# Kernel tuning notes

Hardware: AMD Instinct MI355X
Metric: run time of the kernel (lower is better)

The kernel has to match this reference:

```python
import jax, jax.numpy as jnp
import numpy as np

H = 16          # n_self_heads
CHUNK = 256     # chunk_size in chunk_gate_retention
GLN = 16.0      # gate_logit_normalizer
EPS = 1e-5      # norm_eps


def _rope_interleaved(t, cos, sin):
    # t: [B,T,H,hd]; cos,sin: [T,hd//2]; interleaved pairs (even, odd)
    x1 = t[..., 0::2]
    x2 = t[..., 1::2]
    c = cos[None, :, None, :]
    s = sin[None, :, None, :]
    r1 = x1 * c - x2 * s
    r2 = x1 * s + x2 * c
    return jnp.stack([r1, r2], axis=-1).reshape(t.shape)


def setup_inputs() -> dict:
    key = jax.random.key(0)
    ks = jax.random.split(key, 8)
    B, T, D = 2, 4096, 2048
    hd = D // H
    sc = D ** -0.5
    x = jax.random.normal(ks[0], (B, T, D), jnp.float32)
    # real rotary tables (interleaved), [T, hd//2]
    inv_freq = 1.0 / (10000.0 ** (np.arange(0, hd, 2, dtype=np.float32) / hd))
    ang = np.outer(np.arange(T, dtype=np.float32), inv_freq)
    cos = jnp.asarray(np.cos(ang))
    sin = jnp.asarray(np.sin(ang))
    Wq = jax.random.normal(ks[1], (D, D), jnp.float32) * sc
    Wk = jax.random.normal(ks[2], (D, D), jnp.float32) * sc
    Wv = jax.random.normal(ks[3], (D, D), jnp.float32) * sc
    Wg = jax.random.normal(ks[4], (D, D), jnp.float32) * sc
    Wgt = jax.random.normal(ks[5], (D, H), jnp.float32) * sc
    Wout = jax.random.normal(ks[6], (D, D), jnp.float32) * sc
    return {"x": x, "cos": cos, "sin": sin, "Wq": Wq, "Wk": Wk, "Wv": Wv,
            "Wg": Wg, "Wgt": Wgt, "Wout": Wout}


def reference(x, cos, sin, Wq, Wk, Wv, Wg, Wgt, Wout):
    B, T, D = x.shape
    hd = D // H
    N = T // CHUNK
    scale = hd ** -0.5

    q = (x @ Wq).reshape(B, T, H, hd)
    k = (x @ Wk).reshape(B, T, H, hd)
    v = (x @ Wv).reshape(B, T, H, hd)
    g = x @ Wg                                   # [B,T,D] swiglu gate
    gt = jax.nn.log_sigmoid(x @ Wgt) / GLN       # [B,T,H] log-decay per head

    q = _rope_interleaved(q, cos, sin)
    k = _rope_interleaved(k, cos, sin)

    # chunk: [B,H,N,C,hd]
    def chunked(t):
        return t.transpose(0, 2, 1, 3).reshape(B, H, N, CHUNK, hd)
    qc, kc, vc = chunked(q), chunked(k), chunked(v)

    gtc = gt.transpose(0, 2, 1).reshape(B, H, N, CHUNK).astype(jnp.float32)
    gcum = jnp.cumsum(gtc, axis=-1)              # inclusive cumsum within chunk

    # intra-chunk: A[i,j] = (q_i.k_j)*scale * exp(gcum_i - gcum_j), j <= i
    mask = jnp.tril(jnp.ones((CHUNK, CHUNK), bool))
    dec = jnp.where(mask, jnp.exp(gcum[..., :, None] - gcum[..., None, :]), 0.0).astype(x.dtype)
    scores = jnp.einsum('bhncd,bhnsd->bhncs', qc * scale, kc) * dec
    o_inner = jnp.einsum('bhncs,bhnsd->bhncd', scores, vc)

    # cross-chunk recurrent state: S <- S*exp(g_total) + (k*exp(g_total-gcum))^T V * scale
    g_tot = gcum[..., -1:]                       # [B,H,N,1]
    k_dec = jnp.exp(g_tot - gcum).astype(x.dtype)
    S_in = jnp.einsum('bhncd,bhnce->bhnde', kc * k_dec[..., None] * scale, vc)  # [B,H,N,hd,hd]
    q_dec = jnp.exp(gcum).astype(x.dtype)        # [B,H,N,C]
    chunk_dec = jnp.exp(gcum[..., -1]).astype(x.dtype)  # [B,H,N]

    def step(S, inp):
        qcn, qd, Sin, cd = inp
        o_cross = jnp.einsum('bhcd,bhde->bhce', qcn * qd[..., None], S)
        S_new = S * cd[..., None, None] + Sin
        return S_new, o_cross

    xs = (jnp.moveaxis(qc, 2, 0), jnp.moveaxis(q_dec, 2, 0),
          jnp.moveaxis(S_in, 2, 0), jnp.moveaxis(chunk_dec, 2, 0))
    S0 = jnp.zeros((B, H, hd, hd), x.dtype)
    _, o_cross = jax.lax.scan(step, S0, xs)      # [N,B,H,C,hd]

    o = o_inner + jnp.moveaxis(o_cross, 0, 2)    # [B,H,N,C,hd]
    # RMSNorm over head_dim, no affine
    o = o * jax.lax.rsqrt(jnp.mean(o * o, axis=-1, keepdims=True) + EPS)
    o = o.reshape(B, H, T, hd).transpose(0, 2, 1, 3).reshape(B, T, D)
    o = jax.nn.silu(g) * o                       # swiglu(g, o)
    return o @ Wout
```

## Files before the change

kernel.cpp:

```cpp
#include <hip/hip_runtime.h>

typedef unsigned short u16;
typedef short bf16x8 __attribute__((ext_vector_type(8)));
typedef unsigned short u16x8 __attribute__((ext_vector_type(8)));
typedef unsigned short u16x4 __attribute__((ext_vector_type(4)));
typedef float f32x4 __attribute__((ext_vector_type(4)));

typedef __attribute__((address_space(1))) void* gas_ptr;
typedef __attribute__((address_space(3))) void* las_ptr;

__device__ __forceinline__ float bf2f(u16 v) {
  unsigned u = ((unsigned)v) << 16;
  return __builtin_bit_cast(float, u);
}
__device__ __forceinline__ u16 f2bf(float f) {
  unsigned u = __builtin_bit_cast(unsigned, f);
  u += 0x7fffu + ((u >> 16) & 1u);
  return (u16)(u >> 16);
}
__device__ __forceinline__ f32x4 mfma16(bf16x8 a, bf16x8 b, f32x4 c) {
  return __builtin_amdgcn_mfma_f32_16x16x32_bf16(a, b, c, 0, 0, 0);
}
__device__ __forceinline__ void gload_lds16(const void* g, void* l) {
  __builtin_amdgcn_global_load_lds((gas_ptr)g, (las_ptr)l, 16, 0, 0);
}

#define SB __builtin_amdgcn_sched_barrier(0)
#define BAR do { SB; __builtin_amdgcn_s_barrier(); SB; } while (0)

__global__ void k_cast(const float* __restrict__ in, u16* __restrict__ out, int n8) {
  int stride = gridDim.x * blockDim.x;
  for (int i = blockIdx.x * blockDim.x + threadIdx.x; i < n8; i += stride) {
    size_t base = (size_t)i * 8;
    f32x4 a = *(const f32x4*)(in + base);
    f32x4 b = *(const f32x4*)(in + base + 4);
    u16x8 o;
    o[0] = f2bf(a[0]); o[1] = f2bf(a[1]); o[2] = f2bf(a[2]); o[3] = f2bf(a[3]);
    o[4] = f2bf(b[0]); o[5] = f2bf(b[1]); o[6] = f2bf(b[2]); o[7] = f2bf(b[3]);
    *(u16x8*)(out + base) = o;
  }
}

__global__ __launch_bounds__(256) void k_wtrans5(const float* __restrict__ W0,
                                                 const float* __restrict__ W1,
                                                 const float* __restrict__ W2,
                                                 const float* __restrict__ W3,
                                                 const float* __restrict__ W4,
                                                 u16* __restrict__ WT) {
  const int K = 2048, N = 2048;
  int z = blockIdx.z;
  const float* W = (z == 0) ? W0 : (z == 1) ? W1 : (z == 2) ? W2 : (z == 3) ? W3 : W4;
  u16* dst = WT + (size_t)z * 4194304;
  int n0 = blockIdx.x * 64, k0 = blockIdx.y * 64;
  int tid = threadIdx.x;
  __shared__ __align__(16) float tf[64][68];
  int r = tid >> 4, c4 = (tid & 15) * 4;
#pragma unroll
  for (int i = 0; i < 4; ++i) {
    int row = r + i * 16;
    f32x4 v = *(const f32x4*)(W + (size_t)(k0 + row) * N + n0 + c4);
    *(f32x4*)&tf[row][c4] = v;
  }
  __syncthreads();
#pragma unroll
  for (int i = 0; i < 2; ++i) {
    int chunk = tid + i * 256;
    int nl = chunk >> 3, c8 = (chunk & 7) * 8;
    u16x8 o;
#pragma unroll
    for (int m = 0; m < 8; ++m) o[m] = f2bf(tf[c8 + m][nl]);
    *(u16x8*)(dst + (size_t)(n0 + nl) * K + k0 + c8) = o;
  }
}

template <int MODE>
__global__ __launch_bounds__(512, 2) void k_gemm2(const u16* __restrict__ A,
                                                  const u16* __restrict__ Bt,
                                                  void* __restrict__ Cp, int M, int N, int K) {
  __shared__ __align__(16) u16 Al[2][2][8192];
  __shared__ __align__(16) u16 Bl[2][2][8192];
  int tid = threadIdx.x, w = tid >> 6, lane = tid & 63, l15 = lane & 15, l4 = lane >> 4;
  int wm = w >> 2, wn = w & 3;
  int nwg = gridDim.x, bid = blockIdx.x;
  int q8 = nwg >> 3;
  int wg = (bid & 7) * q8 + (bid >> 3);
  int nbx = N >> 8;
  int nstx = nbx >> 2;
  int st = wg >> 4, r16 = wg & 15;
  int sm = st / nstx, sn = st - sm * nstx;
  int m0 = ((sm << 2) + (r16 >> 2)) << 8;
  int n0 = ((sn << 2) + (r16 & 3)) << 8;
  int rA0, rA1, rB0, rB1, cc0, cc1;
  {
    int rr[2], cch[2];
#pragma unroll
    for (int q = 0; q < 2; ++q) {
      int L = (q * 512 + tid) * 16;
      int sub = L >> 10, inner = L & 1023;
      inner ^= ((inner >> 9) & 1) << 5;
      rr[q] = ((sub >> 1) << 4) + (inner >> 6);
      cch[q] = ((sub & 1) << 5) + ((inner & 63) >> 1);
    }
    rA0 = ((rr[0] >> 6) << 7) + (rr[0] & 63);
    rA1 = ((rr[1] >> 6) << 7) + (rr[1] & 63);
    rB0 = ((rr[0] >> 5) << 6) + (rr[0] & 31);
    rB1 = ((rr[1] >> 5) << 6) + (rr[1] & 31);
    cc0 = cch[0]; cc1 = cch[1];
  }
  int innerA = ((l15 << 6) + (l4 << 4)) ^ ((l15 & 8) << 2);
  int ldsW = w << 9;

#define STAGE_A(t, h)                                                                   \
  do {                                                                                  \
    int b_ = (t) & 1;                                                                   \
    gload_lds16(A + (size_t)(m0 + rA0 + (h) * 64) * K + (t) * 64 + cc0, &Al[b_][h][ldsW]); \
    gload_lds16(A + (size_t)(m0 + rA1 + (h) * 64) * K + (t) * 64 + cc1, &Al[b_][h][4096 + ldsW]); \
  } while (0)
#define STAGE_B(t, h)                                                                   \
  do {                                                                                  \
    int b_ = (t) & 1;                                                                   \
    gload_lds16(Bt + (size_t)(n0 + rB0 + (h) * 32) * K + (t) * 64 + cc0, &Bl[b_][h][ldsW]); \
    gload_lds16(Bt + (size_t)(n0 + rB1 + (h) * 32) * K + (t) * 64 + cc1, &Bl[b_][h][4096 + ldsW]); \
  } while (0)

  const f32x4 z4 = {0.f, 0.f, 0.f, 0.f};
  f32x4 acc[8][4];
#pragma unroll
  for (int i = 0; i < 8; ++i)
#pragma unroll
    for (int j = 0; j < 4; ++j) acc[i][j] = z4;
  bf16x8 af0[4][2], af1[4][2], bf0[2][2], bf1[2][2];

#define LDA0(buf)                                                                        \
  do {                                                                                   \
    const char* Ab = (const char*)&Al[buf][0][0];                                        \
    _Pragma("unroll") for (int fi = 0; fi < 4; ++fi) _Pragma("unroll") for (int ks = 0; ks < 2; ++ks) \
        af0[fi][ks] = *(const bf16x8*)(Ab + (((wm * 4 + fi) * 2 + ks) << 10) + innerA);  \
  } while (0)
#define LDA1(buf)                                                                        \
  do {                                                                                   \
    const char* Ab = (const char*)&Al[buf][1][0];                                        \
    _Pragma("unroll") for (int fi = 0; fi < 4; ++fi) _Pragma("unroll") for (int ks = 0; ks < 2; ++ks) \
        af1[fi][ks] = *(const bf16x8*)(Ab + (((wm * 4 + fi) * 2 + ks) << 10) + innerA);  \
  } while (0)
#define LDB0(buf)                                                                        \
  do {                                                                                   \
    const char* Bb = (const char*)&Bl[buf][0][0];                                        \
    _Pragma("unroll") for (int fj = 0; fj < 2; ++fj) _Pragma("unroll") for (int ks = 0; ks < 2; ++ks) \
        bf0[fj][ks] = *(const bf16x8*)(Bb + (((wn * 2 + fj) * 2 + ks) << 10) + innerA);  \
  } while (0)
#define LDB1(buf)                                                                        \
  do {                                                                                   \
    const char* Bb = (const char*)&Bl[buf][1][0];                                        \
    _Pragma("unroll") for (int fj = 0; fj < 2; ++fj) _Pragma("unroll") for (int ks = 0; ks < 2; ++ks) \
        bf1[fj][ks] = *(const bf16x8*)(Bb + (((wn * 2 + fj) * 2 + ks) << 10) + innerA);  \
  } while (0)
#define MM(hm, hn, AF, BF)                                                               \
  do {                                                                                   \
    __builtin_amdgcn_s_setprio(1);                                                       \
    _Pragma("unroll") for (int fi = 0; fi < 4; ++fi) _Pragma("unroll") for (int fj = 0; fj < 2; ++fj) \
        _Pragma("unroll") for (int ks = 0; ks < 2; ++ks)                                 \
            acc[(hm) * 4 + fi][(hn) * 2 + fj] =                                          \
                mfma16(AF[fi][ks], BF[fj][ks], acc[(hm) * 4 + fi][(hn) * 2 + fj]);       \
    __builtin_amdgcn_s_setprio(0);                                                       \
  } while (0)

  int nt = K >> 6;
  STAGE_A(0, 0); STAGE_B(0, 0); STAGE_A(0, 1); STAGE_B(0, 1);
  if (nt > 1) {
    STAGE_A(1, 0); STAGE_B(1, 0);
    asm volatile("s_waitcnt vmcnt(4)" ::: "memory");
  } else {
    asm volatile("s_waitcnt vmcnt(0)" ::: "memory");
  }
  SB;
  BAR;
  LDA0(0); LDB0(0);
  for (int t = 0; t < nt; ++t) {
    int cur = t & 1, nxt = cur ^ 1;
    LDB1(cur);
    if (t + 1 < nt) STAGE_B(t + 1, 1);
    asm volatile("s_waitcnt lgkmcnt(4)" ::: "memory"); SB;
    MM(0, 0, af0, bf0);
    BAR;
    LDA1(cur);
    if (t + 1 < nt) STAGE_A(t + 1, 1);
    asm volatile("s_waitcnt lgkmcnt(8)" ::: "memory"); SB;
    MM(0, 1, af0, bf1);
    BAR;
    if (t + 2 < nt) STAGE_A(t + 2, 0);
    asm volatile("s_waitcnt lgkmcnt(0)" ::: "memory"); SB;
    MM(1, 0, af1, bf0);
    if (t + 1 < nt) {
      if (t + 2 < nt) { asm volatile("s_waitcnt vmcnt(6)" ::: "memory"); }
      else            { asm volatile("s_waitcnt vmcnt(4)" ::: "memory"); }
    } else            { asm volatile("s_waitcnt vmcnt(0)" ::: "memory"); }
    SB;
    BAR;
    if (t + 1 < nt) { LDA0(nxt); LDB0(nxt); }
    if (t + 2 < nt) STAGE_B(t + 2, 0);
    MM(1, 1, af1, bf1);
    BAR;
  }
  asm volatile("s_waitcnt lgkmcnt(0)" ::: "memory");
  asm volatile("s_waitcnt vmcnt(0)" ::: "memory");
#undef STAGE_A
#undef STAGE_B
#undef LDA0
#undef LDA1
#undef LDB0
#undef LDB1
#undef MM
#pragma unroll
  for (int fi = 0; fi < 8; ++fi)
#pragma unroll
    for (int fj = 0; fj < 4; ++fj) {
      int row = m0 + wm * 128 + fi * 16 + l4 * 4;
      int col = n0 + wn * 64 + fj * 16 + l15;
      if (MODE == 1) {
        float* C = (float*)Cp;
#pragma unroll
        for (int reg = 0; reg < 4; ++reg) C[(size_t)(row + reg) * N + col] = acc[fi][fj][reg];
      } else {
        u16* C = (u16*)Cp + (size_t)(col >> 11) * 16777216 + (col & 2047);
#pragma unroll
        for (int reg = 0; reg < 4; ++reg) C[(size_t)(row + reg) * 2048] = f2bf(acc[fi][fj][reg]);
      }
    }
}

__global__ __launch_bounds__(256) void k_gt(const float* __restrict__ x, const float* __restrict__ Wgt,
                                            float* __restrict__ gt) {
  int t = blockIdx.x, tid = threadIdx.x;
  __shared__ __align__(16) float xs[2048];
#pragma unroll
  for (int i = 0; i < 8; ++i) xs[tid + i * 256] = x[(size_t)t * 2048 + tid + i * 256];
  __syncthreads();
  int head = tid & 15, ks = tid >> 4;
  float p = 0.f;
  for (int i = 0; i < 128; ++i) {
    int k = ks + i * 16;
    p += xs[k] * Wgt[k * 16 + head];
  }
  __shared__ float ps[16][17];
  ps[ks][head] = p;
  __syncthreads();
  if (tid < 16) {
    float z = 0.f;
#pragma unroll
    for (int j = 0; j < 16; ++j) z += ps[j][tid];
    float lsz = (z >= 0.f) ? -log1pf(__expf(-z)) : (z - log1pf(__expf(z)));
    int b = t >> 12, tl = t & 4095;
    gt[((size_t)(b * 16 + tid)) * 4096 + tl] = lsz * 0.0625f;
  }
}

__global__ void k_cumsum(const float* __restrict__ gt, float* __restrict__ gcum) {
  int n = blockIdx.x, bh = blockIdx.y, c = threadIdx.x;
  __shared__ float s[256];
  size_t base = (size_t)bh * 4096 + n * 256;
  s[c] = gt[base + c];
  __syncthreads();
  for (int off = 1; off < 256; off <<= 1) {
    float t = (c >= off) ? s[c - off] : 0.f;
    __syncthreads();
    s[c] += t;
    __syncthreads();
  }
  gcum[base + c] = s[c];
}

__global__ void k_rope(u16* __restrict__ q, u16* __restrict__ k,
                       const float* __restrict__ cosT, const float* __restrict__ sinT) {
  const size_t total = (size_t)8192 * 512;
  size_t stride = (size_t)gridDim.x * blockDim.x;
  for (size_t idx = (size_t)blockIdx.x * blockDim.x + threadIdx.x; idx < total; idx += stride) {
    size_t tok = idx >> 9;
    int g4 = (int)(idx & 511);
    int col = g4 * 4;
    int i0 = (col & 127) >> 1;
    int tl = (int)(tok & 4095);
    float c0 = cosT[tl * 64 + i0], s0 = sinT[tl * 64 + i0];
    float c1 = cosT[tl * 64 + i0 + 1], s1 = sinT[tl * 64 + i0 + 1];
    size_t base = tok * 2048 + col;
    u16x4 qv = *(u16x4*)(q + base);
    float a0 = bf2f(qv[0]), a1 = bf2f(qv[1]), a2 = bf2f(qv[2]), a3 = bf2f(qv[3]);
    u16x4 qo;
    qo[0] = f2bf(a0 * c0 - a1 * s0); qo[1] = f2bf(a0 * s0 + a1 * c0);
    qo[2] = f2bf(a2 * c1 - a3 * s1); qo[3] = f2bf(a2 * s1 + a3 * c1);
    *(u16x4*)(q + base) = qo;
    u16x4 kv = *(u16x4*)(k + base);
    float b0 = bf2f(kv[0]), b1 = bf2f(kv[1]), b2 = bf2f(kv[2]), b3 = bf2f(kv[3]);
    u16x4 ko;
    ko[0] = f2bf(b0 * c0 - b1 * s0); ko[1] = f2bf(b0 * s0 + b1 * c0);
    ko[2] = f2bf(b2 * c1 - b3 * s1); ko[3] = f2bf(b2 * s1 + b3 * c1);
    *(u16x4*)(k + base) = ko;
  }
}

__global__ __launch_bounds__(256) void k_sin(const u16* __restrict__ kb, const u16* __restrict__ vb,
                                             const float* __restrict__ gcum, float* __restrict__ SinT) {
  int n = blockIdx.x, bh = blockIdx.y;
  int b = bh >> 4, h = bh & 15;
  int tid = threadIdx.x, w = tid >> 6, lane = tid & 63, l15 = lane & 15, l4 = lane >> 4;
  size_t t0 = (size_t)b * 4096 + n * 256;
  __shared__ float gc[256];
  __shared__ __align__(16) u16 kt[128 * 72];
  __shared__ __align__(16) u16 vt[128 * 72];
  gc[tid] = gcum[(size_t)bh * 4096 + n * 256 + tid];
  __syncthreads();
  float gtot = gc[255];
  const float scale = 0.08838834764831845f;
  const f32x4 z4 = {0.f, 0.f, 0.f, 0.f};
  f32x4 acc[2][8];
#pragma unroll
  for (int i = 0; i < 2; ++i)
#pragma unroll
    for (int j = 0; j < 8; ++j) acc[i][j] = z4;
  int cl = tid >> 2, fq = (tid & 3) * 32;
  for (int c0 = 0; c0 < 256; c0 += 64) {
    __syncthreads();
    float kd = __expf(gtot - gc[c0 + cl]) * scale;
    const u16* kp = kb + (t0 + c0 + cl) * 2048 + h * 128 + fq;
    const u16* vp = vb + (t0 + c0 + cl) * 2048 + h * 128 + fq;
#pragma unroll
    for (int jj = 0; jj < 4; ++jj) {
      u16x8 kv = *(const u16x8*)(kp + jj * 8);
      u16x8 vv = *(const u16x8*)(vp + jj * 8);
#pragma unroll
      for (int m = 0; m < 8; ++m) {
        int f = fq + jj * 8 + m;
        kt[f * 72 + cl] = f2bf(bf2f(kv[m]) * kd);
        vt[f * 72 + cl] = vv[m];
      }
    }
    __syncthreads();
#pragma unroll
    for (int ks = 0; ks < 2; ++ks) {
      int coff = ks * 32 + l4 * 8;
      bf16x8 bfr[8];
#pragma unroll
      for (int bc = 0; bc < 8; ++bc) bfr[bc] = *(const bf16x8*)(vt + (bc * 16 + l15) * 72 + coff);
#pragma unroll
      for (int ar = 0; ar < 2; ++ar) {
        bf16x8 afr = *(const bf16x8*)(kt + (w * 32 + ar * 16 + l15) * 72 + coff);
#pragma unroll
        for (int bc = 0; bc < 8; ++bc) acc[ar][bc] = mfma16(afr, bfr[bc], acc[ar][bc]);
      }
    }
  }
  size_t sbo = ((size_t)bh * 16 + n) * 16384;
#pragma unroll
  for (int ar = 0; ar < 2; ++ar) {
    int d = w * 32 + ar * 16 + l4 * 4;
#pragma unroll
    for (int bc = 0; bc < 8; ++bc) {
      int e = bc * 16 + l15;
      *(f32x4*)(SinT + sbo + (size_t)e * 128 + d) = acc[ar][bc];
    }
  }
}

__global__ void k_state(const float* __restrict__ SinT, const float* __restrict__ gcum,
                        u16* __restrict__ S_T) {
  int bh = blockIdx.x >> 3, sl = blockIdx.x & 7;
  int base_l = sl * 2048 + threadIdx.x;
  float S[8];
#pragma unroll
  for (int i = 0; i < 8; ++i) S[i] = 0.f;
  for (int nn = 0; nn < 16; ++nn) {
    size_t tb = ((size_t)bh * 16 + nn) * 16384;
#pragma unroll
    for (int i = 0; i < 8; ++i) S_T[tb + base_l + i * 256] = f2bf(S[i]);
    float cd = __expf(gcum[(size_t)bh * 4096 + nn * 256 + 255]);
#pragma unroll
    for (int i = 0; i < 8; ++i) S[i] = S[i] * cd + SinT[tb + base_l + i * 256];
  }
}

__global__ __launch_bounds__(512, 4) void k_attn(
    const u16* __restrict__ qb, const u16* __restrict__ kb, const u16* __restrict__ vb,
    const u16* __restrict__ gbuf, const float* __restrict__ gcum,
    const u16* __restrict__ S_T, u16* __restrict__ ob) {
  int n = blockIdx.x, bh = blockIdx.y;
  int b = bh >> 4, h = bh & 15;
  int tid = threadIdx.x, w = tid >> 6, lane = tid & 63, l15 = lane & 15, l4 = lane >> 4;
  size_t t0 = (size_t)b * 4096 + n * 256;
  __shared__ float gc[256];
  __shared__ __align__(16) u16 vt[32768];
  __shared__ __align__(16) u16 Pb[8][512];
  if (tid < 256) gc[tid] = gcum[(size_t)bh * 4096 + n * 256 + tid];
  {
    int s = tid & 255, e0 = (tid >> 8) * 64;
    const u16* vp = vb + (t0 + s) * 2048 + h * 128 + e0;
#pragma unroll
    for (int j = 0; j < 8; ++j) {
      u16x8 vv = *(const u16x8*)(vp + j * 8);
#pragma unroll
      for (int m = 0; m < 8; ++m) {
        int e = e0 + j * 8 + m;
        vt[(e * 256 + s) ^ ((e & 7) << 3)] = vv[m];
      }
    }
  }
  __syncthreads();
  const float scale = 0.08838834764831845f;
  u16* P = Pb[w];
  const f32x4 z4 = {0.f, 0.f, 0.f, 0.f};
  f32x4 acc[2][8];
#pragma unroll
  for (int i = 0; i < 2; ++i)
#pragma unroll
    for (int j = 0; j < 8; ++j) acc[i][j] = z4;
  int r0s[2], nsbs[2];
  r0s[0] = w * 16;        nsbs[0] = (w + 2) >> 1;
  r0s[1] = (15 - w) * 16; nsbs[1] = 8 - (w >> 1);
#pragma unroll
  for (int rb = 0; rb < 2; ++rb) {
    int r0 = r0s[rb], nsb = nsbs[rb];
    bf16x8 qa[4];
    {
      const u16* qp = qb + (t0 + r0 + l15) * 2048 + h * 128 + l4 * 8;
#pragma unroll
      for (int ks = 0; ks < 4; ++ks) qa[ks] = *(const bf16x8*)(qp + ks * 32);
    }
    for (int sbk = 0; sbk < nsb; ++sbk) {
      int s0 = sbk * 32;
      f32x4 sc[2] = {z4, z4};
#pragma unroll
      for (int cf = 0; cf < 2; ++cf) {
        const u16* kp = kb + (t0 + s0 + cf * 16 + l15) * 2048 + h * 128 + l4 * 8;
#pragma unroll
        for (int ks = 0; ks < 4; ++ks)
          sc[cf] = mfma16(qa[ks], *(const bf16x8*)(kp + ks * 32), sc[cf]);
      }
#pragma unroll
      for (int cf = 0; cf < 2; ++cf) {
        int s = s0 + cf * 16 + l15;
        float gs = gc[s];
#pragma unroll
        for (int reg = 0; reg < 4; ++reg) {
          int rl = l4 * 4 + reg;
          int r = r0 + rl;
          float val = (r >= s) ? sc[cf][reg] * scale * __expf(gc[r] - gs) : 0.f;
          P[(rl * 32 + cf * 16 + l15) ^ ((rl & 3) << 3)] = f2bf(val);
        }
      }
      bf16x8 pa = *(const bf16x8*)(P + ((l15 * 32 + l4 * 8) ^ ((l15 & 3) << 3)));
#pragma unroll
      for (int bc = 0; bc < 8; ++bc) {
        int e = bc * 16 + l15;
        bf16x8 vf = *(const bf16x8*)(vt + ((e * 256 + s0 + l4 * 8) ^ ((e & 7) << 3)));
        acc[rb][bc] = mfma16(pa, vf, acc[rb][bc]);
      }
    }
  }
  size_t sbase = ((size_t)bh * 16 + n) * 16384;
#pragma unroll
  for (int rb = 0; rb < 2; ++rb) {
    int r0 = r0s[rb];
    float qd = __expf(gc[r0 + l15]);
#pragma unroll
    for (int ks = 0; ks < 4; ++ks) {
      u16x8 qu = *(const u16x8*)(qb + (t0 + r0 + l15) * 2048 + h * 128 + ks * 32 + l4 * 8);
      u16x8 ru;
#pragma unroll
      for (int m = 0; m < 8; ++m) ru[m] = f2bf(bf2f(qu[m]) * qd);
      bf16x8 pa2 = __builtin_bit_cast(bf16x8, ru);
#pragma unroll
      for (int bc = 0; bc < 8; ++bc) {
        int e = bc * 16 + l15;
        bf16x8 sf = *(const bf16x8*)(S_T + sbase + (size_t)e * 128 + ks * 32 + l4 * 8);
        acc[rb][bc] = mfma16(pa2, sf, acc[rb][bc]);
      }
    }
  }
#pragma unroll
  for (int rb = 0; rb < 2; ++rb) {
    int r0 = r0s[rb];
#pragma unroll
    for (int reg = 0; reg < 4; ++reg) {
      float ss = 0.f;
#pragma unroll
      for (int bc = 0; bc < 8; ++bc) { float v = acc[rb][bc][reg]; ss += v * v; }
      ss += __shfl_xor(ss, 1);
      ss += __shfl_xor(ss, 2);
      ss += __shfl_xor(ss, 4);
      ss += __shfl_xor(ss, 8);
      float rinv = rsqrtf(ss * 0.0078125f + 1e-5f);
      int r = r0 + l4 * 4 + reg;
      size_t rowoff = (t0 + r) * 2048 + h * 128;
#pragma unroll
      for (int bc = 0; bc < 8; ++bc) {
        int e = bc * 16 + l15;
        float gval = bf2f(gbuf[rowoff + e]);
        float sig = 1.f / (1.f + __expf(-gval));
        ob[rowoff + e] = f2bf(acc[rb][bc][reg] * rinv * gval * sig);
      }
    }
  }
}

extern "C" void kernel_launch(void* const* d_in, const int* in_sizes, int n_in,
                              void* d_out, int out_size, void* d_ws, size_t ws_size,
                              hipStream_t stream) {
  const float* x    = (const float*)d_in[0];
  const float* cosT = (const float*)d_in[1];
  const float* sinT = (const float*)d_in[2];
  const float* Wq   = (const float*)d_in[3];
  const float* Wk   = (const float*)d_in[4];
  const float* Wv   = (const float*)d_in[5];
  const float* Wg   = (const float*)d_in[6];
  const float* Wgt  = (const float*)d_in[7];
  const float* Wout = (const float*)d_in[8];
  float* out = (float*)d_out;

  const size_t MB32 = (size_t)33554432;
  const size_t W8   = (size_t)8388608;
  char* ws = (char*)d_ws;
  size_t need = MB32 + 5 * W8 + 4 * MB32 + 2 * (size_t)524288;
  if (ws_size < need) return;

  u16*   xb    = (u16*)(ws);
  float* SinT  = (float*)(ws);
  u16*   ob    = (u16*)(ws);
  u16*   WqT   = (u16*)(ws + MB32);
  u16*   S_T   = (u16*)(ws + MB32);
  u16*   WoutT = (u16*)(ws + MB32 + 4 * W8);
  u16*   qb    = (u16*)(ws + MB32 + 5 * W8);
  u16*   kb    = qb + 16777216;
  u16*   vb    = qb + 2 * 16777216;
  u16*   gb    = qb + 3 * (size_t)16777216;
  float* gt    = (float*)(ws + MB32 + 5 * W8 + 4 * MB32);
  float* gcum  = (float*)(ws + MB32 + 5 * W8 + 4 * MB32 + 524288);

  k_cast<<<2048, 256, 0, stream>>>(x, xb, 2097152);
  k_wtrans5<<<dim3(32, 32, 5), 256, 0, stream>>>(Wq, Wk, Wv, Wg, Wout, WqT);

  k_gemm2<2><<<1024, 512, 0, stream>>>(xb, WqT, qb, 8192, 8192, 2048);

  k_gt<<<8192, 256, 0, stream>>>(x, Wgt, gt);
  k_cumsum<<<dim3(16, 32), 256, 0, stream>>>(gt, gcum);
  k_rope<<<4096, 256, 0, stream>>>(qb, kb, cosT, sinT);
  k_sin<<<dim3(16, 32), 256, 0, stream>>>(kb, vb, gcum, SinT);
  k_state<<<256, 256, 0, stream>>>(SinT, gcum, S_T);
  k_attn<<<dim3(16, 32), 512, 0, stream>>>(qb, kb, vb, gb, gcum, S_T, ob);
  k_gemm2<1><<<256, 512, 0, stream>>>(ob, WoutT, out, 8192, 2048, 2048);
}
```

Baseline: 545.4 us.

## Split LDS fragment loads into halves to deepen GEMM software pipeline

Replaces the whole-fragment LDS load macros with half-granularity loads, so the A fragments are fetched in two halves spread across the MFMA phases. The global-to-LDS staging order and the vmcnt/lgkmcnt wait counts are rescheduled to match. The aim is to hide LDS read latency behind MFMA work and cut stalls at barriers. The hand-tuned waitcnt values carry a risk of races or of more stalls if they are miscounted.

```diff
diff --git a/kernel.cpp b/kernel.cpp
--- a/kernel.cpp
+++ b/kernel.cpp
@@ -131,29 +131,19 @@
     for (int j = 0; j < 4; ++j) acc[i][j] = z4;
   bf16x8 af0[4][2], af1[4][2], bf0[2][2], bf1[2][2];
 
-#define LDA0(buf)                                                                        \
+#define LDA_H(AF, buf, hh, fi0, fi1)                                                     \
   do {                                                                                   \
-    const char* Ab = (const char*)&Al[buf][0][0];                                        \
-    _Pragma("unroll") for (int fi = 0; fi < 4; ++fi) _Pragma("unroll") for (int ks = 0; ks < 2; ++ks) \
-        af0[fi][ks] = *(const bf16x8*)(Ab + (((wm * 4 + fi) * 2 + ks) << 10) + innerA);  \
+    const char* Ab = (const char*)&Al[buf][hh][0];                                       \
+    _Pragma("unroll") for (int fi = (fi0); fi < (fi1); ++fi)                             \
+        _Pragma("unroll") for (int ks = 0; ks < 2; ++ks)                                 \
+            AF[fi][ks] = *(const bf16x8*)(Ab + (((wm * 4 + fi) * 2 + ks) << 10) + innerA); \
   } while (0)
-#define LDA1(buf)                                                                        \
+#define LDB_H(BF, buf, hh)                                                               \
   do {                                                                                   \
-    const char* Ab = (const char*)&Al[buf][1][0];                                        \
-    _Pragma("unroll") for (int fi = 0; fi < 4; ++fi) _Pragma("unroll") for (int ks = 0; ks < 2; ++ks) \
-        af1[fi][ks] = *(const bf16x8*)(Ab + (((wm * 4 + fi) * 2 + ks) << 10) + innerA);  \
-  } while (0)
-#define LDB0(buf)                                                                        \
-  do {                                                                                   \
-    const char* Bb = (const char*)&Bl[buf][0][0];                                        \
-    _Pragma("unroll") for (int fj = 0; fj < 2; ++fj) _Pragma("unroll") for (int ks = 0; ks < 2; ++ks) \
-        bf0[fj][ks] = *(const bf16x8*)(Bb + (((wn * 2 + fj) * 2 + ks) << 10) + innerA);  \
-  } while (0)
-#define LDB1(buf)                                                                        \
-  do {                                                                                   \
-    const char* Bb = (const char*)&Bl[buf][1][0];                                        \
-    _Pragma("unroll") for (int fj = 0; fj < 2; ++fj) _Pragma("unroll") for (int ks = 0; ks < 2; ++ks) \
-        bf1[fj][ks] = *(const bf16x8*)(Bb + (((wn * 2 + fj) * 2 + ks) << 10) + innerA);  \
+    const char* Bb = (const char*)&Bl[buf][hh][0];                                       \
+    _Pragma("unroll") for (int fj = 0; fj < 2; ++fj)                                     \
+        _Pragma("unroll") for (int ks = 0; ks < 2; ++ks)                                 \
+            BF[fj][ks] = *(const bf16x8*)(Bb + (((wn * 2 + fj) * 2 + ks) << 10) + innerA); \
   } while (0)
 #define MM(hm, hn, AF, BF)                                                               \
   do {                                                                                   \
@@ -166,7 +156,7 @@
   } while (0)
 
   int nt = K >> 6;
-  STAGE_A(0, 0); STAGE_B(0, 0); STAGE_A(0, 1); STAGE_B(0, 1);
+  STAGE_A(0, 0); STAGE_B(0, 0); STAGE_B(0, 1); STAGE_A(0, 1);
   if (nt > 1) {
     STAGE_A(1, 0); STAGE_B(1, 0);
     asm volatile("s_waitcnt vmcnt(4)" ::: "memory");
@@ -175,29 +165,30 @@
   }
   SB;
   BAR;
-  LDA0(0); LDB0(0);
+  LDA_H(af0, 0, 0, 0, 2); LDA_H(af0, 0, 0, 2, 4); LDB_H(bf0, 0, 0);
   for (int t = 0; t < nt; ++t) {
     int cur = t & 1, nxt = cur ^ 1;
-    LDB1(cur);
+    LDB_H(bf1, cur, 1); LDA_H(af1, cur, 1, 0, 2);
     if (t + 1 < nt) STAGE_B(t + 1, 1);
-    asm volatile("s_waitcnt lgkmcnt(4)" ::: "memory"); SB;
+    asm volatile("s_waitcnt lgkmcnt(8)" ::: "memory"); SB;
     MM(0, 0, af0, bf0);
     BAR;
-    LDA1(cur);
+    LDA_H(af1, cur, 1, 2, 4);
     if (t + 1 < nt) STAGE_A(t + 1, 1);
     asm volatile("s_waitcnt lgkmcnt(8)" ::: "memory"); SB;
     MM(0, 1, af0, bf1);
-    BAR;
-    if (t + 2 < nt) STAGE_A(t + 2, 0);
-    asm volatile("s_waitcnt lgkmcnt(0)" ::: "memory"); SB;
-    MM(1, 0, af1, bf0);
-    if (t + 1 < nt) {
-      if (t + 2 < nt) { asm volatile("s_waitcnt vmcnt(6)" ::: "memory"); }
-      else            { asm volatile("s_waitcnt vmcnt(4)" ::: "memory"); }
-    } else            { asm volatile("s_waitcnt vmcnt(0)" ::: "memory"); }
+    if (t + 1 < nt) { asm volatile("s_waitcnt vmcnt(4)" ::: "memory"); }
+    else            { asm volatile("s_waitcnt vmcnt(0)" ::: "memory"); }
     SB;
     BAR;
-    if (t + 1 < nt) { LDA0(nxt); LDB0(nxt); }
+    if (t + 1 < nt) LDA_H(af0, nxt, 0, 0, 2);
+    if (t + 2 < nt) STAGE_A(t + 2, 0);
+    if (t + 1 < nt) { asm volatile("s_waitcnt lgkmcnt(4)" ::: "memory"); }
+    else            { asm volatile("s_waitcnt lgkmcnt(0)" ::: "memory"); }
+    SB;
+    MM(1, 0, af1, bf0);
+    BAR;
+    if (t + 1 < nt) { LDA_H(af0, nxt, 0, 2, 4); LDB_H(bf0, nxt, 0); }
     if (t + 2 < nt) STAGE_B(t + 2, 0);
     MM(1, 1, af1, bf1);
     BAR;
@@ -206,10 +197,8 @@
   asm volatile("s_waitcnt vmcnt(0)" ::: "memory");
 #undef STAGE_A
 #undef STAGE_B
-#undef LDA0
-#undef LDA1
-#undef LDB0
-#undef LDB1
+#undef LDA_H
+#undef LDB_H
 #undef MM
 #pragma unroll
   for (int fi = 0; fi < 8; ++fi)
```

New measurement: 548.6 us. No clear change (+0.6%).

## Fuse RoPE into QKV GEMM epilogue and merge cast with gate-logit kernel

Applied to the files above, without the earlier changes.

Applies rotary embedding to q and k inside the projection GEMM's store epilogue, using a lane shuffle to fetch the paired column, which removes the separate k_rope pass over q and k. Also merges the fp32-to-bf16 cast of x with the log-decay gate projection, handling four tokens per block so x is read once and each Wgt load is reused. Costs are extra cos/sin loads and shuffles in the GEMM epilogue and scalar (non-vectorised) bf16 stores in the cast. Rounding now happens once after the rotation instead of before and after it, so the bf16 values differ slightly.

```diff
diff --git a/kernel.cpp b/kernel.cpp
--- a/kernel.cpp
+++ b/kernel.cpp
@@ -28,16 +28,50 @@
 #define SB __builtin_amdgcn_sched_barrier(0)
 #define BAR do { SB; __builtin_amdgcn_s_barrier(); SB; } while (0)
 
-__global__ void k_cast(const float* __restrict__ in, u16* __restrict__ out, int n8) {
-  int stride = gridDim.x * blockDim.x;
-  for (int i = blockIdx.x * blockDim.x + threadIdx.x; i < n8; i += stride) {
-    size_t base = (size_t)i * 8;
-    f32x4 a = *(const f32x4*)(in + base);
-    f32x4 b = *(const f32x4*)(in + base + 4);
-    u16x8 o;
-    o[0] = f2bf(a[0]); o[1] = f2bf(a[1]); o[2] = f2bf(a[2]); o[3] = f2bf(a[3]);
-    o[4] = f2bf(b[0]); o[5] = f2bf(b[1]); o[6] = f2bf(b[2]); o[7] = f2bf(b[3]);
-    *(u16x8*)(out + base) = o;
+__global__ __launch_bounds__(256) void k_gtcast(const float* __restrict__ x,
+                                                const float* __restrict__ Wgt,
+                                                u16* __restrict__ xb,
+                                                float* __restrict__ gt) {
+  int t0 = blockIdx.x * 4;
+  int tid = threadIdx.x;
+  __shared__ __align__(16) float xs[4][2048];
+#pragma unroll
+  for (int tok = 0; tok < 4; ++tok) {
+    size_t rb = (size_t)(t0 + tok) * 2048;
+#pragma unroll
+    for (int i = 0; i < 8; ++i) {
+      int idx = tid + i * 256;
+      float v = x[rb + idx];
+      xs[tok][idx] = v;
+      xb[rb + idx] = f2bf(v);
+    }
+  }
+  __syncthreads();
+  int head = tid & 15, ks = tid >> 4;
+  float p0 = 0.f, p1 = 0.f, p2 = 0.f, p3 = 0.f;
+  for (int i = 0; i < 128; ++i) {
+    int k = ks + i * 16;
+    float wv = Wgt[k * 16 + head];
+    p0 += xs[0][k] * wv;
+    p1 += xs[1][k] * wv;
+    p2 += xs[2][k] * wv;
+    p3 += xs[3][k] * wv;
+  }
+  __shared__ float ps[4][16][17];
+  ps[0][ks][head] = p0;
+  ps[1][ks][head] = p1;
+  ps[2][ks][head] = p2;
+  ps[3][ks][head] = p3;
+  __syncthreads();
+  if (tid < 64) {
+    int tok = tid >> 4, hh = tid & 15;
+    float z = 0.f;
+#pragma unroll
+    for (int j = 0; j < 16; ++j) z += ps[tok][j][hh];
+    float lsz = (z >= 0.f) ? -log1pf(__expf(-z)) : (z - log1pf(__expf(z)));
+    int t = t0 + tok;
+    int b = t >> 12, tl = t & 4095;
+    gt[((size_t)(b * 16 + hh)) * 4096 + tl] = lsz * 0.0625f;
   }
 }
 
@@ -76,7 +110,9 @@
 template <int MODE>
 __global__ __launch_bounds__(512, 2) void k_gemm2(const u16* __restrict__ A,
                                                   const u16* __restrict__ Bt,
-                                                  void* __restrict__ Cp, int M, int N, int K) {
+                                                  void* __restrict__ Cp, int M, int N, int K,
+                                                  const float* __restrict__ cosT,
+                                                  const float* __restrict__ sinT) {
   __shared__ __align__(16) u16 Al[2][2][8192];
   __shared__ __align__(16) u16 Bl[2][2][8192];
   int tid = threadIdx.x, w = tid >> 6, lane = tid & 63, l15 = lane & 15, l4 = lane >> 4;
@@ -215,44 +251,33 @@
   for (int fi = 0; fi < 8; ++fi)
 #pragma unroll
     for (int fj = 0; fj < 4; ++fj) {
-      int row = m0 + wm * 128 + fi * 16 + l4 * 4;
+      int row0 = m0 + wm * 128 + fi * 16 + l4 * 4;
       int col = n0 + wn * 64 + fj * 16 + l15;
       if (MODE == 1) {
         float* C = (float*)Cp;
 #pragma unroll
-        for (int reg = 0; reg < 4; ++reg) C[(size_t)(row + reg) * N + col] = acc[fi][fj][reg];
+        for (int reg = 0; reg < 4; ++reg) C[(size_t)(row0 + reg) * N + col] = acc[fi][fj][reg];
       } else {
-        u16* C = (u16*)Cp + (size_t)(col >> 11) * 16777216 + (col & 2047);
-#pragma unroll
-        for (int reg = 0; reg < 4; ++reg) C[(size_t)(row + reg) * 2048] = f2bf(acc[fi][fj][reg]);
-      }
-    }
-}
-
-__global__ __launch_bounds__(256) void k_gt(const float* __restrict__ x, const float* __restrict__ Wgt,
-                                            float* __restrict__ gt) {
-  int t = blockIdx.x, tid = threadIdx.x;
-  __shared__ __align__(16) float xs[2048];
-#pragma unroll
-  for (int i = 0; i < 8; ++i) xs[tid + i * 256] = x[(size_t)t * 2048 + tid + i * 256];
-  __syncthreads();
-  int head = tid & 15, ks = tid >> 4;
-  float p = 0.f;
-  for (int i = 0; i < 128; ++i) {
-    int k = ks + i * 16;
-    p += xs[k] * Wgt[k * 16 + head];
-  }
-  __shared__ float ps[16][17];
-  ps[ks][head] = p;
-  __syncthreads();
-  if (tid < 16) {
-    float z = 0.f;
-#pragma unroll
-    for (int j = 0; j < 16; ++j) z += ps[j][tid];
-    float lsz = (z >= 0.f) ? -log1pf(__expf(-z)) : (z - log1pf(__expf(z)));
-    int b = t >> 12, tl = t & 4095;
-    gt[((size_t)(b * 16 + tid)) * 4096 + tl] = lsz * 0.0625f;
-  }
+        int bufi = col >> 11;
+        u16* C = (u16*)Cp + (size_t)bufi * 16777216 + (col & 2047);
+        if (bufi < 2) {
+          int i0 = (col & 127) >> 1;
+          bool evenc = (col & 1) == 0;
+#pragma unroll
+          for (int reg = 0; reg < 4; ++reg) {
+            int tl = (row0 + reg) & 4095;
+            float cv = cosT[tl * 64 + i0], sv = sinT[tl * 64 + i0];
+            float v = acc[fi][fj][reg];
+            float partner = __shfl_xor(v, 1);
+            float r = evenc ? (v * cv - partner * sv) : (partner * sv + v * cv);
+            C[(size_t)(row0 + reg) * 2048] = f2bf(r);
+          }
+        } else {
+#pragma unroll
+          for (int reg = 0; reg < 4; ++reg) C[(size_t)(row0 + reg) * 2048] = f2bf(acc[fi][fj][reg]);
+        }
+      }
+    }
 }
 
 __global__ void k_cumsum(const float* __restrict__ gt, float* __restrict__ gcum) {
@@ -268,34 +293,6 @@
     __syncthreads();
   }
   gcum[base + c] = s[c];
-}
-
-__global__ void k_rope(u16* __restrict__ q, u16* __restrict__ k,
-                       const float* __restrict__ cosT, const float* __restrict__ sinT) {
-  const size_t total = (size_t)8192 * 512;
-  size_t stride = (size_t)gridDim.x * blockDim.x;
-  for (size_t idx = (size_t)blockIdx.x * blockDim.x + threadIdx.x; idx < total; idx += stride) {
-    size_t tok = idx >> 9;
-    int g4 = (int)(idx & 511);
-    int col = g4 * 4;
-    int i0 = (col & 127) >> 1;
-    int tl = (int)(tok & 4095);
-    float c0 = cosT[tl * 64 + i0], s0 = sinT[tl * 64 + i0];
-    float c1 = cosT[tl * 64 + i0 + 1], s1 = sinT[tl * 64 + i0 + 1];
-    size_t base = tok * 2048 + col;
-    u16x4 qv = *(u16x4*)(q + base);
-    float a0 = bf2f(qv[0]), a1 = bf2f(qv[1]), a2 = bf2f(qv[2]), a3 = bf2f(qv[3]);
-    u16x4 qo;
-    qo[0] = f2bf(a0 * c0 - a1 * s0); qo[1] = f2bf(a0 * s0 + a1 * c0);
-    qo[2] = f2bf(a2 * c1 - a3 * s1); qo[3] = f2bf(a2 * s1 + a3 * c1);
-    *(u16x4*)(q + base) = qo;
-    u16x4 kv = *(u16x4*)(k + base);
-    float b0 = bf2f(kv[0]), b1 = bf2f(kv[1]), b2 = bf2f(kv[2]), b3 = bf2f(kv[3]);
-    u16x4 ko;
-    ko[0] = f2bf(b0 * c0 - b1 * s0); ko[1] = f2bf(b0 * s0 + b1 * c0);
-    ko[2] = f2bf(b2 * c1 - b3 * s1); ko[3] = f2bf(b2 * s1 + b3 * c1);
-    *(u16x4*)(k + base) = ko;
-  }
 }
 
 __global__ __launch_bounds__(256) void k_sin(const u16* __restrict__ kb, const u16* __restrict__ vb,
@@ -534,16 +531,14 @@
   float* gt    = (float*)(ws + MB32 + 5 * W8 + 4 * MB32);
   float* gcum  = (float*)(ws + MB32 + 5 * W8 + 4 * MB32 + 524288);
 
-  k_cast<<<2048, 256, 0, stream>>>(x, xb, 2097152);
+  k_gtcast<<<2048, 256, 0, stream>>>(x, Wgt, xb, gt);
   k_wtrans5<<<dim3(32, 32, 5), 256, 0, stream>>>(Wq, Wk, Wv, Wg, Wout, WqT);
 
-  k_gemm2<2><<<1024, 512, 0, stream>>>(xb, WqT, qb, 8192, 8192, 2048);
-
-  k_gt<<<8192, 256, 0, stream>>>(x, Wgt, gt);
+  k_gemm2<2><<<1024, 512, 0, stream>>>(xb, WqT, qb, 8192, 8192, 2048, cosT, sinT);
+
   k_cumsum<<<dim3(16, 32), 256, 0, stream>>>(gt, gcum);
-  k_rope<<<4096, 256, 0, stream>>>(qb, kb, cosT, sinT);
   k_sin<<<dim3(16, 32), 256, 0, stream>>>(kb, vb, gcum, SinT);
   k_state<<<256, 256, 0, stream>>>(SinT, gcum, S_T);
   k_attn<<<dim3(16, 32), 512, 0, stream>>>(qb, kb, vb, gb, gcum, S_T, ob);
-  k_gemm2<1><<<256, 512, 0, stream>>>(ob, WoutT, out, 8192, 2048, 2048);
-}
+  k_gemm2<1><<<256, 512, 0, stream>>>(ob, WoutT, out, 8192, 2048, 2048, nullptr, nullptr);
+}
```

Result: faster. 497.4 us (-8.8%).
